# Kernel tuning notes

Hardware: AMD Instinct MI355X
Metric: run time of the kernel (lower is better)

## Reference

```python
import jax, jax.numpy as jnp
import numpy as np


def swish(x):
    return x * jax.nn.sigmoid(x)


def setup_inputs() -> dict:
    key = jax.random.key(0)
    ks = jax.random.split(key, 10)
    N, E, R, H = 50000, 300000, 6, 512
    return {
        "x": jax.random.randint(ks[0], (N,), 0, 95),
        "rbf": jax.random.normal(ks[1], (E, R), dtype=jnp.float32),
        "i": jax.random.randint(ks[2], (E,), 0, N),
        "j": jax.random.randint(ks[3], (E,), 0, N),
        "emb_weight": jax.random.normal(ks[4], (95, H), dtype=jnp.float32),
        "W_rbf0": jax.random.normal(ks[5], (R, H), dtype=jnp.float32) * 0.1,
        "b_rbf0": jax.random.normal(ks[6], (H,), dtype=jnp.float32) * 0.1,
        "W_lin": jax.random.normal(ks[7], (3 * H, H), dtype=jnp.float32) * 0.02,
        "b_lin": jax.random.normal(ks[8], (H,), dtype=jnp.float32) * 0.1,
        "W_rbf1": jax.random.normal(ks[9], (R, H), dtype=jnp.float32) * 0.1,
    }


def reference(x, rbf, i, j, emb_weight, W_rbf0, b_rbf0, W_lin, b_lin, W_rbf1):
    # node embedding lookup: [N, H]
    h = emb_weight[x]
    # radial basis projection + swish: [E, H]
    rbf0 = swish(rbf @ W_rbf0 + b_rbf0)
    # gather endpoints, concat, linear, swish: [E, H]
    cat = jnp.concatenate([h[i], h[j], rbf0], axis=-1)  # [E, 3H]
    e1 = swish(cat @ W_lin + b_lin)
    # bias-free rbf projection, elementwise product: [E, H]
    e2 = (rbf @ W_rbf1) * e1
    return (e1, e2)
```

## Files before the change

### kernel.cpp

```cpp
#include <hip/hip_runtime.h>
#include <hip/hip_bf16.h>

typedef __attribute__((ext_vector_type(8))) short short8;
typedef __attribute__((ext_vector_type(4))) float f32x4;

#define NQ 95
#define HDIM 512
#define RBF 6
#define BM 64

static __device__ __forceinline__ unsigned short f2bf(float f){
  unsigned u = __float_as_uint(f);
  u += 0x7FFF + ((u >> 16) & 1);
  return (unsigned short)(u >> 16);
}
static __device__ __forceinline__ float swishf(float z){
  float e = __expf(-z);
  return z * __builtin_amdgcn_rcpf(1.0f + e);
}

__global__ __launch_bounds__(512) void prep_tables(
    const float* __restrict__ emb, const float* __restrict__ W_lin,
    const float* __restrict__ b_lin, float* __restrict__ P0,
    float* __restrict__ P1)
{
  __shared__ float sE[HDIM];
  const int v   = blockIdx.x % NQ;
  const int tab = blockIdx.x / NQ;
  const int t   = threadIdx.x;
  sE[t] = emb[v*HDIM + t];
  __syncthreads();
  const float* W = W_lin + (size_t)tab * HDIM * HDIM + t;
  float a = tab ? 0.f : b_lin[t];
  #pragma unroll 8
  for (int k = 0; k < HDIM; ++k)
    a += sE[k] * W[(size_t)k * HDIM];
  (tab ? P1 : P0)[v*HDIM + t] = a;
}

__global__ __launch_bounds__(256) void prep_w2t(
    const float* __restrict__ W_lin, unsigned short* __restrict__ W2T)
{
  const int idx = blockIdx.x * 256 + threadIdx.x;
  const int n  = idx >> 6;
  const int kb = (idx & 63) * 8;
  const float* W2 = W_lin + (size_t)1024 * HDIM;
  unsigned p[4];
  #pragma unroll
  for (int c = 0; c < 4; ++c){
    unsigned lo = f2bf(W2[(size_t)(kb + 2*c    ) * HDIM + n]);
    unsigned hi = f2bf(W2[(size_t)(kb + 2*c + 1) * HDIM + n]);
    p[c] = lo | (hi << 16);
  }
  uint4 o; o.x = p[0]; o.y = p[1]; o.z = p[2]; o.w = p[3];
  *(uint4*)(W2T + (size_t)n * HDIM + kb) = o;
}

__global__ __launch_bounds__(1024, 4) void fused_edge(
    const int* __restrict__ xv, const float* __restrict__ rbf,
    const int* __restrict__ ei, const int* __restrict__ ej,
    const float* __restrict__ W0, const float* __restrict__ b0,
    const float* __restrict__ W1,
    const float* __restrict__ P0, const float* __restrict__ P1,
    const unsigned short* __restrict__ W2T,
    float* __restrict__ out, int E)
{
  __shared__ unsigned short sA[BM * HDIM];
  __shared__ float sRbf[BM * RBF];
  __shared__ int sXi[BM], sXj[BM];

  const int t  = threadIdx.x;
  const int eb = blockIdx.x * BM;
  const int me = min(BM, E - eb);

  if (t < 96){
    float4 v = make_float4(0.f, 0.f, 0.f, 0.f);
    size_t gi  = (size_t)eb * RBF + (size_t)t * 4;
    size_t lim = (size_t)E * RBF;
    if (gi + 4 <= lim) v = *(const float4*)(rbf + gi);
    else {
      float* pv = (float*)&v;
      for (int c = 0; c < 4; ++c) if (gi + c < lim) pv[c] = rbf[gi + c];
    }
    *(float4*)(sRbf + t*4) = v;
  } else if (t >= 128 && t < 192){
    int q = t - 128;
    int xi = 0, xj = 0;
    int e = eb + q;
    if (e < E){ xi = xv[ei[e]]; xj = xv[ej[e]]; }
    sXi[q] = xi; sXj[q] = xj;
  }

  const int cp = t & 255;
  const int q4 = t >> 8;
  float2 w0c[RBF];
  #pragma unroll
  for (int r = 0; r < RBF; ++r) w0c[r] = *(const float2*)(W0 + r*HDIM + 2*cp);
  float2 bb = *(const float2*)(b0 + 2*cp);

  __syncthreads();

  char* sAb = (char*)sA;
  {
    const int swz_t = 4 * cp;
    const int m0 = q4 * 16;
    #pragma unroll 2
    for (int mm = 0; mm < 16; ++mm){
      const int m = m0 + mm;
      float2 ra = *(const float2*)(sRbf + m*RBF);
      float2 rb = *(const float2*)(sRbf + m*RBF + 2);
      float2 rc = *(const float2*)(sRbf + m*RBF + 4);
      float z0 = bb.x, z1 = bb.y;
      z0 += ra.x*w0c[0].x + ra.y*w0c[1].x + rb.x*w0c[2].x
          + rb.y*w0c[3].x + rc.x*w0c[4].x + rc.y*w0c[5].x;
      z1 += ra.x*w0c[0].y + ra.y*w0c[1].y + rb.x*w0c[2].y
          + rb.y*w0c[3].y + rc.x*w0c[4].y + rc.y*w0c[5].y;
      unsigned pk = (unsigned)f2bf(swishf(z0)) | ((unsigned)f2bf(swishf(z1)) << 16);
      *(unsigned*)(sAb + (m*1024 + (swz_t ^ ((m & 7) << 4)))) = pk;
    }
  }
  __syncthreads();

  const int lane  = t & 63;
  const int w     = t >> 6;
  const int nbase = w * 32;
  const int rlo   = lane & 15;
  const int kg    = lane >> 4;

  f32x4 acc[4][2];
  #pragma unroll
  for (int a = 0; a < 4; ++a)
    #pragma unroll
    for (int b = 0; b < 2; ++b) acc[a][b] = f32x4{0.f, 0.f, 0.f, 0.f};

  const unsigned short* bp0 = W2T + (size_t)(nbase      + rlo)*HDIM + kg*8;
  const unsigned short* bp1 = bp0 + (size_t)16*HDIM;

  #pragma unroll 4
  for (int ks = 0; ks < 16; ++ks){
    short8 b0r = *(const short8*)(bp0 + ks*32);
    short8 b1r = *(const short8*)(bp1 + ks*32);
    short8 af[4];
    #pragma unroll
    for (int mt = 0; mt < 4; ++mt){
      int row = mt*16 + rlo;
      int off = row*1024 + ((ks*64 + kg*16) ^ ((row & 7) << 4));
      af[mt] = *(const short8*)(sAb + off);
    }
    #pragma unroll
    for (int mt = 0; mt < 4; ++mt){
      acc[mt][0] = __builtin_amdgcn_mfma_f32_16x16x32_bf16(af[mt], b0r, acc[mt][0], 0, 0, 0);
      acc[mt][1] = __builtin_amdgcn_mfma_f32_16x16x32_bf16(af[mt], b1r, acc[mt][1], 0, 0, 0);
    }
  }

  float w1c[RBF][2];
  #pragma unroll
  for (int nt = 0; nt < 2; ++nt){
    int n = nbase + nt*16 + rlo;
    #pragma unroll
    for (int r = 0; r < RBF; ++r) w1c[r][nt] = W1[r*HDIM + n];
  }

  float* __restrict__ out2 = out + (size_t)E * HDIM;
  #pragma unroll
  for (int mt = 0; mt < 4; ++mt){
    #pragma unroll
    for (int r = 0; r < 4; ++r){
      const int m  = mt*16 + kg*4 + r;
      const bool valid = (m < me);
      const int xi = sXi[m], xj = sXj[m];
      const float* p0row = P0 + (size_t)xi * HDIM;
      const float* p1row = P1 + (size_t)xj * HDIM;
      const size_t orow = (size_t)(eb + m) * HDIM;
      float2 ra = *(const float2*)(sRbf + m*RBF);
      float2 rb = *(const float2*)(sRbf + m*RBF + 2);
      float2 rc = *(const float2*)(sRbf + m*RBF + 4);
      #pragma unroll
      for (int nt = 0; nt < 2; ++nt){
        const int n = nbase + nt*16 + rlo;
        float f  = acc[mt][nt][r] + p0row[n] + p1row[n];
        float e1 = swishf(f);
        float g  = ra.x*w1c[0][nt] + ra.y*w1c[1][nt] + rb.x*w1c[2][nt]
                 + rb.y*w1c[3][nt] + rc.x*w1c[4][nt] + rc.y*w1c[5][nt];
        if (valid){
          __builtin_nontemporal_store(e1,   out  + orow + n);
          __builtin_nontemporal_store(g*e1, out2 + orow + n);
        }
      }
    }
  }
}

extern "C" void kernel_launch(void* const* d_in, const int* in_sizes, int n_in,
                              void* d_out, int out_size, void* d_ws, size_t ws_size,
                              hipStream_t stream) {
  const int*   xv    = (const int*)  d_in[0];
  const float* rbf   = (const float*)d_in[1];
  const int*   ei    = (const int*)  d_in[2];
  const int*   ej    = (const int*)  d_in[3];
  const float* emb   = (const float*)d_in[4];
  const float* W0    = (const float*)d_in[5];
  const float* b0    = (const float*)d_in[6];
  const float* W_lin = (const float*)d_in[7];
  const float* b_lin = (const float*)d_in[8];
  const float* W1    = (const float*)d_in[9];
  float* out = (float*)d_out;

  const int E = in_sizes[2];

  float* P0 = (float*)d_ws;
  float* P1 = P0 + NQ * HDIM;
  unsigned short* W2T = (unsigned short*)(P1 + NQ * HDIM);

  prep_tables<<<2 * NQ, 512, 0, stream>>>(emb, W_lin, b_lin, P0, P1);
  prep_w2t<<<(HDIM * (HDIM/8)) / 256, 256, 0, stream>>>(W_lin, W2T);

  const int nblk = (E + BM - 1) / BM;
  fused_edge<<<nblk, 1024, 0, stream>>>(xv, rbf, ei, ej, W0, b0, W1,
                                        P0, P1, W2T, out, E);
}
```

Measured before the change: 572.9 us.

## Split edge tile across two 512-thread blocks and stage outputs through LDS

Each 64-edge tile is now handled by two 512-thread blocks, each computing half of the output columns, and the shared rbf0 A-tile is built by both. The epilogue writes e1/e2 into padded shared memory and then emits coalesced 16-byte row stores instead of scattered scalar nontemporal stores. This aims to improve store coalescing and scheduling flexibility, at the cost of computing the rbf0 tile twice, extra barriers, and dropping nontemporal hints.

```diff
diff --git a/kernel.cpp b/kernel.cpp
--- a/kernel.cpp
+++ b/kernel.cpp
@@ -8,6 +8,7 @@
 #define HDIM 512
 #define RBF 6
 #define BM 64
+#define SFS 264
 
 static __device__ __forceinline__ unsigned short f2bf(float f){
   unsigned u = __float_as_uint(f);
@@ -56,7 +57,7 @@
   *(uint4*)(W2T + (size_t)n * HDIM + kb) = o;
 }
 
-__global__ __launch_bounds__(1024, 4) void fused_edge(
+__global__ __launch_bounds__(512, 4) void fused_edge(
     const int* __restrict__ xv, const float* __restrict__ rbf,
     const int* __restrict__ ei, const int* __restrict__ ej,
     const float* __restrict__ W0, const float* __restrict__ b0,
@@ -69,9 +70,11 @@
   __shared__ float sRbf[BM * RBF];
   __shared__ int sXi[BM], sXj[BM];
 
-  const int t  = threadIdx.x;
-  const int eb = blockIdx.x * BM;
-  const int me = min(BM, E - eb);
+  const int t     = threadIdx.x;
+  const int tile  = blockIdx.x >> 1;
+  const int nhalf = blockIdx.x & 1;
+  const int eb    = tile * BM;
+  const int me    = min(BM, E - eb);
 
   if (t < 96){
     float4 v = make_float4(0.f, 0.f, 0.f, 0.f);
@@ -91,8 +94,8 @@
     sXi[q] = xi; sXj[q] = xj;
   }
 
-  const int cp = t & 255;
-  const int q4 = t >> 8;
+  const int cp   = t & 255;
+  const int half = t >> 8;
   float2 w0c[RBF];
   #pragma unroll
   for (int r = 0; r < RBF; ++r) w0c[r] = *(const float2*)(W0 + r*HDIM + 2*cp);
@@ -103,9 +106,9 @@
   char* sAb = (char*)sA;
   {
     const int swz_t = 4 * cp;
-    const int m0 = q4 * 16;
+    const int m0 = half * 32;
     #pragma unroll 2
-    for (int mm = 0; mm < 16; ++mm){
+    for (int mm = 0; mm < 32; ++mm){
       const int m = m0 + mm;
       float2 ra = *(const float2*)(sRbf + m*RBF);
       float2 rb = *(const float2*)(sRbf + m*RBF + 2);
@@ -123,70 +126,84 @@
 
   const int lane  = t & 63;
   const int w     = t >> 6;
-  const int nbase = w * 32;
+  const int ncol0 = w * 32;
   const int rlo   = lane & 15;
   const int kg    = lane >> 4;
 
   f32x4 acc[4][2];
   #pragma unroll
-  for (int a = 0; a < 4; ++a)
-    #pragma unroll
-    for (int b = 0; b < 2; ++b) acc[a][b] = f32x4{0.f, 0.f, 0.f, 0.f};
-
-  const unsigned short* bp0 = W2T + (size_t)(nbase      + rlo)*HDIM + kg*8;
+  for (int a = 0; a < 4; ++a){
+    acc[a][0] = f32x4{0.f,0.f,0.f,0.f};
+    acc[a][1] = f32x4{0.f,0.f,0.f,0.f};
+  }
+
+  const unsigned short* bp0 = W2T + (size_t)(nhalf*256 + ncol0 + rlo)*HDIM + kg*8;
   const unsigned short* bp1 = bp0 + (size_t)16*HDIM;
 
-  #pragma unroll 4
   for (int ks = 0; ks < 16; ++ks){
     short8 b0r = *(const short8*)(bp0 + ks*32);
     short8 b1r = *(const short8*)(bp1 + ks*32);
-    short8 af[4];
     #pragma unroll
     for (int mt = 0; mt < 4; ++mt){
       int row = mt*16 + rlo;
       int off = row*1024 + ((ks*64 + kg*16) ^ ((row & 7) << 4));
-      af[mt] = *(const short8*)(sAb + off);
-    }
-    #pragma unroll
-    for (int mt = 0; mt < 4; ++mt){
-      acc[mt][0] = __builtin_amdgcn_mfma_f32_16x16x32_bf16(af[mt], b0r, acc[mt][0], 0, 0, 0);
-      acc[mt][1] = __builtin_amdgcn_mfma_f32_16x16x32_bf16(af[mt], b1r, acc[mt][1], 0, 0, 0);
-    }
-  }
-
+      short8 af = *(const short8*)(sAb + off);
+      acc[mt][0] = __builtin_amdgcn_mfma_f32_16x16x32_bf16(af, b0r, acc[mt][0], 0, 0, 0);
+      acc[mt][1] = __builtin_amdgcn_mfma_f32_16x16x32_bf16(af, b1r, acc[mt][1], 0, 0, 0);
+    }
+  }
+
+  __syncthreads();
+
+  float* sE1 = (float*)sA;
+  float* sE2 = sE1 + 16*SFS;
   float w1c[RBF][2];
   #pragma unroll
   for (int nt = 0; nt < 2; ++nt){
-    int n = nbase + nt*16 + rlo;
-    #pragma unroll
-    for (int r = 0; r < RBF; ++r) w1c[r][nt] = W1[r*HDIM + n];
-  }
-
+    const int ng = nhalf*256 + ncol0 + nt*16 + rlo;
+    #pragma unroll
+    for (int r = 0; r < RBF; ++r) w1c[r][nt] = W1[r*HDIM + ng];
+  }
+
+  const int c4 = lane * 4;
+  const int gs = nhalf*256 + c4;
   float* __restrict__ out2 = out + (size_t)E * HDIM;
-  #pragma unroll
-  for (int mt = 0; mt < 4; ++mt){
+
+  #pragma unroll
+  for (int c = 0; c < 4; ++c){
+    if (c) __syncthreads();
     #pragma unroll
     for (int r = 0; r < 4; ++r){
-      const int m  = mt*16 + kg*4 + r;
-      const bool valid = (m < me);
-      const int xi = sXi[m], xj = sXj[m];
-      const float* p0row = P0 + (size_t)xi * HDIM;
-      const float* p1row = P1 + (size_t)xj * HDIM;
-      const size_t orow = (size_t)(eb + m) * HDIM;
+      const int m  = c*16 + kg*4 + r;
+      const int lr = kg*4 + r;
+      const float* p0row = P0 + (size_t)sXi[m] * HDIM;
+      const float* p1row = P1 + (size_t)sXj[m] * HDIM;
       float2 ra = *(const float2*)(sRbf + m*RBF);
       float2 rb = *(const float2*)(sRbf + m*RBF + 2);
       float2 rc = *(const float2*)(sRbf + m*RBF + 4);
       #pragma unroll
       for (int nt = 0; nt < 2; ++nt){
-        const int n = nbase + nt*16 + rlo;
-        float f  = acc[mt][nt][r] + p0row[n] + p1row[n];
+        const int nl = ncol0 + nt*16 + rlo;
+        const int ng = nhalf*256 + nl;
+        float f  = acc[c][nt][r] + p0row[ng] + p1row[ng];
         float e1 = swishf(f);
         float g  = ra.x*w1c[0][nt] + ra.y*w1c[1][nt] + rb.x*w1c[2][nt]
                  + rb.y*w1c[3][nt] + rc.x*w1c[4][nt] + rc.y*w1c[5][nt];
-        if (valid){
-          __builtin_nontemporal_store(e1,   out  + orow + n);
-          __builtin_nontemporal_store(g*e1, out2 + orow + n);
-        }
+        sE1[lr*SFS + nl] = e1;
+        sE2[lr*SFS + nl] = g * e1;
+      }
+    }
+    __syncthreads();
+    #pragma unroll
+    for (int j = 0; j < 2; ++j){
+      const int lr = j*8 + w;
+      const int m  = c*16 + lr;
+      if (m < me){
+        const size_t orow = (size_t)(eb + m) * HDIM + gs;
+        f32x4 v1 = *(const f32x4*)(sE1 + lr*SFS + c4);
+        *(f32x4*)(out  + orow) = v1;
+        f32x4 v2 = *(const f32x4*)(sE2 + lr*SFS + c4);
+        *(f32x4*)(out2 + orow) = v2;
       }
     }
   }
@@ -217,6 +234,6 @@
   prep_w2t<<<(HDIM * (HDIM/8)) / 256, 256, 0, stream>>>(W_lin, W2T);
 
   const int nblk = (E + BM - 1) / BM;
-  fused_edge<<<nblk, 1024, 0, stream>>>(xv, rbf, ei, ej, W0, b0, W1,
-                                        P0, P1, W2T, out, E);
-}
+  fused_edge<<<2 * nblk, 512, 0, stream>>>(xv, rbf, ei, ej, W0, b0, W1,
+                                           P0, P1, W2T, out, E);
+}
```

Result: slower. 593.5 us (+3.6%).
